# Kernel optimization log

Measured on AMD Instinct MI355X. Metric: run time of the kernel, lower is better.

The kernel has to match this reference:

```python
import jax, jax.numpy as jnp
import numpy as np

HIDDEN = 32
N_BLOCKS = 2


def setup_inputs() -> dict:
    key = jax.random.key(0)
    ks = jax.random.split(key, 8)
    B, S, F = 256, 4096, 8
    H = HIDDEN
    inp = {
        "x": jax.random.normal(ks[0], (B, S, F), dtype=jnp.float32),
        # embed
        "W_embed": jax.random.normal(ks[1], (F, H), dtype=jnp.float32) * (F ** -0.5),
        "b_embed": jnp.zeros((H,), jnp.float32),
        # per-block selective-SSM params (stacked over blocks)
        "W_delta": jax.random.normal(ks[2], (N_BLOCKS, H, H), dtype=jnp.float32) * (H ** -0.5),
        "b_delta": jnp.zeros((N_BLOCKS, H), jnp.float32),
        "A_log": jnp.log(jnp.broadcast_to(jnp.arange(1, H + 1, dtype=jnp.float32), (N_BLOCKS, H))),
        "W_gate": jax.random.normal(ks[3], (N_BLOCKS, H, H), dtype=jnp.float32) * (H ** -0.5),
        "b_gate": jnp.zeros((N_BLOCKS, H), jnp.float32),
        # head: LayerNorm + MLP
        "ln_gamma": jnp.ones((H,), jnp.float32),
        "ln_beta": jnp.zeros((H,), jnp.float32),
        "W1": jax.random.normal(ks[4], (H, H), dtype=jnp.float32) * (H ** -0.5),
        "b1": jnp.zeros((H,), jnp.float32),
        "W2": jax.random.normal(ks[5], (H, 1), dtype=jnp.float32) * (H ** -0.5),
        "b2": jnp.zeros((1,), jnp.float32),
    }
    return inp


def _ssm_block(h, Wd, bd, A_log, Wg, bg):
    """Diagonal selective SSM: input-dependent decay, gated output, residual."""
    # h: [B, S, H]
    delta = jax.nn.softplus(jnp.einsum('bsh,hk->bsk', h, Wd) + bd)  # [B,S,H]
    abar = jnp.exp(delta * (-jnp.exp(A_log)))                       # [B,S,H] in (0,1)
    xin = delta * h                                                 # [B,S,H]

    def step(s, ab_xi):
        ab, xi = ab_xi
        s = ab * s + xi
        return s, s

    B, S, H = h.shape
    s0 = jnp.zeros((B, H), h.dtype)
    # scan over time (axis S), vectorized over batch & channels
    _, states = jax.lax.scan(step, s0, (abar.transpose(1, 0, 2), xin.transpose(1, 0, 2)))
    states = states.transpose(1, 0, 2)  # [B,S,H]
    gate = jax.nn.sigmoid(jnp.einsum('bsh,hk->bsk', h, Wg) + bg)
    return h + states * gate


def reference(x, W_embed, b_embed, W_delta, b_delta, A_log, W_gate, b_gate,
              ln_gamma, ln_beta, W1, b1, W2, b2):
    h = jnp.einsum('bsf,fh->bsh', x, W_embed) + b_embed  # [B,S,H]
    for i in range(N_BLOCKS):
        h = _ssm_block(h, W_delta[i], b_delta[i], A_log[i], W_gate[i], b_gate[i])
    hl = h[:, -1, :]  # [B,H] last timestep
    mu = jnp.mean(hl, axis=-1, keepdims=True)
    var = jnp.mean((hl - mu) ** 2, axis=-1, keepdims=True)
    hn = (hl - mu) / jnp.sqrt(var + 1e-5) * ln_gamma + ln_beta
    z = jax.nn.gelu(hn @ W1 + b1)
    return (z @ W2 + b2).squeeze(-1)  # [B]
```

## Files before the change

kernel.cpp:

```cpp
#include <hip/hip_runtime.h>
#include <math.h>

#define BB 256
#define SS 4096
#define FF 8
#define HH 32
#define TT 256
#define NT (SS/TT)
#define NTHREADS 1024
#define NG 16
#define CL 16
#define SUB 8

#define L2E  1.4426950408889634f
#define LN2f 0.6931471805599453f

typedef _Float16 half2v __attribute__((ext_vector_type(2)));
typedef __fp16   pk16   __attribute__((ext_vector_type(2)));

__device__ __forceinline__ float fexp2(float x){
#if __has_builtin(__builtin_amdgcn_exp2f)
    return __builtin_amdgcn_exp2f(x);
#else
    return exp2f(x);
#endif
}
__device__ __forceinline__ float flog2(float x){
#if __has_builtin(__builtin_amdgcn_logf)
    return __builtin_amdgcn_logf(x);
#else
    return log2f(x);
#endif
}
__device__ __forceinline__ float frcp(float x){
#if __has_builtin(__builtin_amdgcn_rcpf)
    return __builtin_amdgcn_rcpf(x);
#else
    return 1.0f/x;
#endif
}
__device__ __forceinline__ float fdot2(half2v a, half2v b, float c){
#if __has_builtin(__builtin_amdgcn_fdot2)
    return __builtin_amdgcn_fdot2(a, b, c, false);
#else
    return c + (float)a.x*(float)b.x + (float)a.y*(float)b.y;
#endif
}
__device__ __forceinline__ half2v bch2(unsigned int u){
    return __builtin_bit_cast(half2v, u);
}

__device__ __forceinline__ float softplus_n(float z){
    const float t = fexp2(-fabsf(z) * L2E);
    return fmaxf(z, 0.f) + LN2f * flog2(1.f + t);
}
__device__ __forceinline__ float sigmoid_n(float z){
    return frcp(1.f + fexp2(-z * L2E));
}

__global__ __launch_bounds__(NTHREADS, 4)
void forecast_fused(const float* __restrict__ x,
                    const float* __restrict__ Wemb, const float* __restrict__ bemb,
                    const float* __restrict__ Wd,   const float* __restrict__ bd,
                    const float* __restrict__ Alog,
                    const float* __restrict__ Wg,   const float* __restrict__ bg,
                    const float* __restrict__ gmma, const float* __restrict__ beta,
                    const float* __restrict__ W1,   const float* __restrict__ b1,
                    const float* __restrict__ W2,   const float* __restrict__ b2,
                    float* __restrict__ out)
{
    __shared__ __align__(16) unsigned int xs16[2][TT][4];
    __shared__ __align__(16) unsigned int h1h[TT][16];
    __shared__ float wdpS[FF][HH];
    __shared__ float wgpS[FF][HH];
    __shared__ float bdpS[HH], bgpS[HH];
    __shared__ float2 cfS[2][NG][HH];
    __shared__ float s1s[2][HH];
    __shared__ float hlast[HH];

    const int tid = threadIdx.x;
    const int c   = tid & (HH - 1);
    const int s   = (tid >> 5) & 1;
    const int g   = tid >> 6;
    const int b   = blockIdx.x;
    const int tsb = g * CL + s * SUB;
    const int xrow = tid >> 2, xdc = tid & 3;

    if (tid < FF * HH) {
        const int f = tid >> 5, cc = tid & 31;
        float accd = 0.f, accg = 0.f;
#pragma unroll
        for (int k = 0; k < HH; ++k) {
            const float w = Wemb[f * HH + k];
            accd += w * Wd[k * HH + cc];
            accg += w * Wg[k * HH + cc];
        }
        wdpS[f][cc] = accd;
        wgpS[f][cc] = accg;
    }
    if (tid < HH) {
        float ad = bd[tid], ag = bg[tid];
#pragma unroll
        for (int k = 0; k < HH; ++k) {
            ad += bemb[k] * Wd[k * HH + tid];
            ag += bemb[k] * Wg[k * HH + tid];
        }
        bdpS[tid] = ad; bgpS[tid] = ag;
        s1s[0][tid] = 0.f;
    }
    __syncthreads();

    half2v weh[FF/2], wdh[FF/2], wgh[FF/2], wh[HH/2];
#pragma unroll
    for (int j = 0; j < FF/2; ++j) {
        half2v a;
        a.x = (_Float16)Wemb[(2*j) * HH + c];   a.y = (_Float16)Wemb[(2*j+1) * HH + c];
        weh[j] = a;
        a.x = (_Float16)wdpS[2*j][c];           a.y = (_Float16)wdpS[2*j+1][c];
        wdh[j] = a;
        a.x = (_Float16)wgpS[2*j][c];           a.y = (_Float16)wgpS[2*j+1][c];
        wgh[j] = a;
    }
#pragma unroll
    for (int j = 0; j < HH/2; ++j) {
        half2v a;
        a.x = (_Float16)Wd[HH * HH + (2*j)   * HH + c];
        a.y = (_Float16)Wd[HH * HH + (2*j+1) * HH + c];
        wh[j] = a;
    }
    const float bec  = bemb[c];
    const float bd1p = bdpS[c], bg1p = bgpS[c], bd2 = bd[HH + c];
    const float nA1 = -expf(Alog[c]) * L2E;
    const float nA2 = -expf(Alog[HH + c]) * L2E;

    float s2v = 0.f;

    {
        const float2 xv = *reinterpret_cast<const float2*>(
            x + ((size_t)b * SS + xrow) * FF + xdc * 2);
        const pk16 pk = __builtin_amdgcn_cvt_pkrtz(xv.x, xv.y);
        xs16[0][xrow][xdc] = __builtin_bit_cast(unsigned int, pk);
    }
    __syncthreads();

    for (int it = 0; it < NT; ++it) {
        const int p = it & 1;

        float2 xnext;
        if (it + 1 < NT)
            xnext = *reinterpret_cast<const float2*>(
                x + ((size_t)b * SS + (it + 1) * TT + xrow) * FF + xdc * 2);

        float prefA[SUB], loc[SUB], gtv[SUB], h0r[SUB], h1r[SUB];
        float sp = 1.f, sl = 0.f;
#pragma unroll
        for (int r = 0; r < SUB; ++r) {
            const int ts = tsb + r;
            const uint4 xq = *reinterpret_cast<const uint4*>(&xs16[p][ts][0]);
            float h0 = bec, zd = bd1p, zg = bg1p;
            h0 = fdot2(bch2(xq.x), weh[0], h0);
            h0 = fdot2(bch2(xq.y), weh[1], h0);
            h0 = fdot2(bch2(xq.z), weh[2], h0);
            h0 = fdot2(bch2(xq.w), weh[3], h0);
            zd = fdot2(bch2(xq.x), wdh[0], zd);
            zd = fdot2(bch2(xq.y), wdh[1], zd);
            zd = fdot2(bch2(xq.z), wdh[2], zd);
            zd = fdot2(bch2(xq.w), wdh[3], zd);
            zg = fdot2(bch2(xq.x), wgh[0], zg);
            zg = fdot2(bch2(xq.y), wgh[1], zg);
            zg = fdot2(bch2(xq.z), wgh[2], zg);
            zg = fdot2(bch2(xq.w), wgh[3], zg);
            const float delta = softplus_n(zd);
            const float ab    = fexp2(delta * nA1);
            sl = ab * sl + delta * h0;
            sp *= ab;
            prefA[r] = sp;
            loc[r]   = sl;
            gtv[r]   = sigmoid_n(zg);
            h0r[r]   = h0;
        }
        const float spO = __shfl_xor(sp, 32);
        const float slO = __shfl_xor(sl, 32);
        if (s) cfS[p][g][c] = make_float2(spO * sp, sp * slO + sl);
        __syncthreads();

        float cy = s1s[p][c];
#pragma unroll
        for (int ch = 0; ch < NG; ++ch) {
            const float2 ax = cfS[p][ch][c];
            const float t = ax.x * cy + ax.y;
            cy = (ch < g) ? t : cy;
        }
        const float ci = s ? (slO + spO * cy) : cy;
        if (g == NG - 1 && s) s1s[p ^ 1][c] = sl + sp * ci;

#pragma unroll
        for (int r = 0; r < SUB; ++r) {
            const float st = loc[r] + prefA[r] * ci;
            const float h1 = h0r[r] + st * gtv[r];
            h1r[r] = h1;
            const float pn = __shfl_xor(h1, 1);
            if (!(c & 1)) {
                const pk16 pk = __builtin_amdgcn_cvt_pkrtz(h1, pn);
                h1h[tsb + r][c >> 1] = __builtin_bit_cast(unsigned int, pk);
            }
        }
        if (it == NT - 1 && g == NG - 1 && s) hlast[c] = h1r[SUB - 1];
        __syncthreads();

        float sp2 = 1.f, sl2 = 0.f;
#pragma unroll
        for (int r = 0; r < SUB; ++r) {
            const uint4* rp = reinterpret_cast<const uint4*>(&h1h[tsb + r][0]);
            const uint4 q0 = rp[0], q1 = rp[1], q2 = rp[2], q3 = rp[3];
            float za = bd2, zb = 0.f;
            za = fdot2(bch2(q0.x), wh[0],  za);
            zb = fdot2(bch2(q0.y), wh[1],  zb);
            za = fdot2(bch2(q0.z), wh[2],  za);
            zb = fdot2(bch2(q0.w), wh[3],  zb);
            za = fdot2(bch2(q1.x), wh[4],  za);
            zb = fdot2(bch2(q1.y), wh[5],  zb);
            za = fdot2(bch2(q1.z), wh[6],  za);
            zb = fdot2(bch2(q1.w), wh[7],  zb);
            za = fdot2(bch2(q2.x), wh[8],  za);
            zb = fdot2(bch2(q2.y), wh[9],  zb);
            za = fdot2(bch2(q2.z), wh[10], za);
            zb = fdot2(bch2(q2.w), wh[11], zb);
            za = fdot2(bch2(q3.x), wh[12], za);
            zb = fdot2(bch2(q3.y), wh[13], zb);
            za = fdot2(bch2(q3.z), wh[14], za);
            zb = fdot2(bch2(q3.w), wh[15], zb);
            const float zd    = za + zb;
            const float delta = softplus_n(zd);
            const float ab    = fexp2(delta * nA2);
            sl2 = ab * sl2 + delta * h1r[r];
            sp2 *= ab;
        }
        const float spO2 = __shfl_xor(sp2, 32);
        const float slO2 = __shfl_xor(sl2, 32);
        if (s) cfS[p][g][c] = make_float2(spO2 * sp2, sp2 * slO2 + sl2);
        if (it + 1 < NT) {
            const pk16 pk = __builtin_amdgcn_cvt_pkrtz(xnext.x, xnext.y);
            xs16[p ^ 1][xrow][xdc] = __builtin_bit_cast(unsigned int, pk);
        }
        __syncthreads();

        if (tid < HH) {
            float cy2 = s2v;
#pragma unroll
            for (int ch = 0; ch < NG; ++ch) {
                const float2 ax = cfS[p][ch][tid];
                cy2 = ax.x * cy2 + ax.y;
            }
            s2v = cy2;
        }
    }
    __syncthreads();

    if (tid < HH) {
        float zg = bg[HH + tid];
#pragma unroll
        for (int k = 0; k < HH; ++k) zg += hlast[k] * Wg[HH * HH + k * HH + tid];
        const float gt2 = sigmoid_n(zg);
        const float h2  = hlast[tid] + s2v * gt2;

        float sum = h2;
#pragma unroll
        for (int m = 1; m < HH; m <<= 1) sum += __shfl_xor(sum, m);
        const float mu = sum * (1.0f / HH);
        const float d  = h2 - mu;
        float vs = d * d;
#pragma unroll
        for (int m = 1; m < HH; m <<= 1) vs += __shfl_xor(vs, m);
        const float rstd = rsqrtf(vs * (1.0f / HH) + 1e-5f);
        const float hn   = d * rstd * gmma[tid] + beta[tid];

        float z = b1[tid];
#pragma unroll
        for (int k = 0; k < HH; ++k) z += __shfl(hn, k) * W1[k * HH + tid];
        const float u  = 2.0f * L2E * 0.7978845608028654f * (z + 0.044715f * z * z * z);
        const float e  = fexp2(u);
        const float th = 1.f - 2.f * frcp(1.f + e);
        const float ge = 0.5f * z * (1.0f + th);
        float v = ge * W2[tid];
#pragma unroll
        for (int m = 1; m < HH; m <<= 1) v += __shfl_xor(v, m);
        if (tid == 0) out[b] = v + b2[0];
    }
}

extern "C" void kernel_launch(void* const* d_in, const int* in_sizes, int n_in,
                              void* d_out, int out_size, void* d_ws, size_t ws_size,
                              hipStream_t stream) {
    const float* x    = (const float*)d_in[0];
    const float* Wemb = (const float*)d_in[1];
    const float* bemb = (const float*)d_in[2];
    const float* Wd   = (const float*)d_in[3];
    const float* bd   = (const float*)d_in[4];
    const float* Alog = (const float*)d_in[5];
    const float* Wg   = (const float*)d_in[6];
    const float* bg   = (const float*)d_in[7];
    const float* gmma = (const float*)d_in[8];
    const float* beta = (const float*)d_in[9];
    const float* W1   = (const float*)d_in[10];
    const float* b1   = (const float*)d_in[11];
    const float* W2   = (const float*)d_in[12];
    const float* b2   = (const float*)d_in[13];
    float* out = (float*)d_out;

    forecast_fused<<<dim3(BB), dim3(NTHREADS), 0, stream>>>(
        x, Wemb, bemb, Wd, bd, Alog, Wg, bg, gmma, beta, W1, b1, W2, b2, out);
}
```

Measured before the change: 181.8 us.

## Use MFMA 16x16x32 for projections and remap wave lanes to channel-time tiles

Replaces the per-thread fdot2 projections (embed, delta, gate, and block-2 delta) with MFMA 16x16x32 f16 instructions, so each wave now handles 16 timesteps for all 32 channels. Each lane holds 4 consecutive timesteps per channel half, and the intra-wave scan combines across lane groups with shuffles. A separate cf2S buffer is added, which removes one barrier per tile because block-2 carries no longer overwrite block-1 carries. The cost is more shuffle traffic and zero-padded MFMA operands, since K is only 8 for the first projections.

```diff
diff --git a/kernel.cpp b/kernel.cpp
--- a/kernel.cpp
+++ b/kernel.cpp
@@ -9,14 +9,14 @@
 #define NT (SS/TT)
 #define NTHREADS 1024
 #define NG 16
-#define CL 16
-#define SUB 8
+#define CLR 16
 
 #define L2E  1.4426950408889634f
 #define LN2f 0.6931471805599453f
 
-typedef _Float16 half2v __attribute__((ext_vector_type(2)));
-typedef __fp16   pk16   __attribute__((ext_vector_type(2)));
+typedef _Float16 f16x8 __attribute__((ext_vector_type(8)));
+typedef float    f32x4 __attribute__((ext_vector_type(4)));
+typedef __fp16   pk16  __attribute__((ext_vector_type(2)));
 
 __device__ __forceinline__ float fexp2(float x){
 #if __has_builtin(__builtin_amdgcn_exp2f)
@@ -38,16 +38,6 @@
 #else
     return 1.0f/x;
 #endif
-}
-__device__ __forceinline__ float fdot2(half2v a, half2v b, float c){
-#if __has_builtin(__builtin_amdgcn_fdot2)
-    return __builtin_amdgcn_fdot2(a, b, c, false);
-#else
-    return c + (float)a.x*(float)b.x + (float)a.y*(float)b.y;
-#endif
-}
-__device__ __forceinline__ half2v bch2(unsigned int u){
-    return __builtin_bit_cast(half2v, u);
 }
 
 __device__ __forceinline__ float softplus_n(float z){
@@ -75,16 +65,20 @@
     __shared__ float wgpS[FF][HH];
     __shared__ float bdpS[HH], bgpS[HH];
     __shared__ float2 cfS[2][NG][HH];
+    __shared__ float2 cf2S[2][NG][HH];
     __shared__ float s1s[2][HH];
     __shared__ float hlast[HH];
 
-    const int tid = threadIdx.x;
-    const int c   = tid & (HH - 1);
-    const int s   = (tid >> 5) & 1;
-    const int g   = tid >> 6;
-    const int b   = blockIdx.x;
-    const int tsb = g * CL + s * SUB;
+    const int tid  = threadIdx.x;
+    const int lane = tid & 63;
+    const int g    = tid >> 6;
+    const int c0   = lane & 15;
+    const int grp  = lane >> 4;
+    const int r0   = grp * 4;
+    const int cb   = g * CLR;
+    const int b    = blockIdx.x;
     const int xrow = tid >> 2, xdc = tid & 3;
+    const int lm16 = (lane - 16) & 63, lm32 = (lane - 32) & 63;
 
     if (tid < FF * HH) {
         const int f = tid >> 5, cc = tid & 31;
@@ -110,28 +104,24 @@
     }
     __syncthreads();
 
-    half2v weh[FF/2], wdh[FF/2], wgh[FF/2], wh[HH/2];
-#pragma unroll
-    for (int j = 0; j < FF/2; ++j) {
-        half2v a;
-        a.x = (_Float16)Wemb[(2*j) * HH + c];   a.y = (_Float16)Wemb[(2*j+1) * HH + c];
-        weh[j] = a;
-        a.x = (_Float16)wdpS[2*j][c];           a.y = (_Float16)wdpS[2*j+1][c];
-        wdh[j] = a;
-        a.x = (_Float16)wgpS[2*j][c];           a.y = (_Float16)wgpS[2*j+1][c];
-        wgh[j] = a;
-    }
-#pragma unroll
-    for (int j = 0; j < HH/2; ++j) {
-        half2v a;
-        a.x = (_Float16)Wd[HH * HH + (2*j)   * HH + c];
-        a.y = (_Float16)Wd[HH * HH + (2*j+1) * HH + c];
-        wh[j] = a;
-    }
-    const float bec  = bemb[c];
-    const float bd1p = bdpS[c], bg1p = bgpS[c], bd2 = bd[HH + c];
-    const float nA1 = -expf(Alog[c]) * L2E;
-    const float nA2 = -expf(Alog[HH + c]) * L2E;
+    f16x8 bh0[2], bzd[2], bzg[2], bwd2[2];
+    float bec[2], bd1p[2], bg1p[2], bd2c[2], nA1[2], nA2[2];
+#pragma unroll
+    for (int q = 0; q < 2; ++q) {
+        const int cq = c0 + 16 * q;
+#pragma unroll
+        for (int j = 0; j < 8; ++j) {
+            bh0[q][j] = (lane < 16) ? (_Float16)Wemb[j * HH + cq] : (_Float16)0.f;
+            bzd[q][j] = (lane < 16) ? (_Float16)wdpS[j][cq]       : (_Float16)0.f;
+            bzg[q][j] = (lane < 16) ? (_Float16)wgpS[j][cq]       : (_Float16)0.f;
+            bwd2[q][j] = (_Float16)Wd[HH * HH + (grp * 8 + j) * HH + cq];
+        }
+        bec[q]  = bemb[cq];
+        bd1p[q] = bdpS[cq]; bg1p[q] = bgpS[cq];
+        bd2c[q] = bd[HH + cq];
+        nA1[q] = -expf(Alog[cq]) * L2E;
+        nA2[q] = -expf(Alog[HH + cq]) * L2E;
+    }
 
     float s2v = 0.f;
 
@@ -146,110 +136,144 @@
     for (int it = 0; it < NT; ++it) {
         const int p = it & 1;
 
-        float2 xnext;
+        float2 xnext = make_float2(0.f, 0.f);
         if (it + 1 < NT)
             xnext = *reinterpret_cast<const float2*>(
                 x + ((size_t)b * SS + (it + 1) * TT + xrow) * FF + xdc * 2);
 
-        float prefA[SUB], loc[SUB], gtv[SUB], h0r[SUB], h1r[SUB];
-        float sp = 1.f, sl = 0.f;
-#pragma unroll
-        for (int r = 0; r < SUB; ++r) {
-            const int ts = tsb + r;
-            const uint4 xq = *reinterpret_cast<const uint4*>(&xs16[p][ts][0]);
-            float h0 = bec, zd = bd1p, zg = bg1p;
-            h0 = fdot2(bch2(xq.x), weh[0], h0);
-            h0 = fdot2(bch2(xq.y), weh[1], h0);
-            h0 = fdot2(bch2(xq.z), weh[2], h0);
-            h0 = fdot2(bch2(xq.w), weh[3], h0);
-            zd = fdot2(bch2(xq.x), wdh[0], zd);
-            zd = fdot2(bch2(xq.y), wdh[1], zd);
-            zd = fdot2(bch2(xq.z), wdh[2], zd);
-            zd = fdot2(bch2(xq.w), wdh[3], zd);
-            zg = fdot2(bch2(xq.x), wgh[0], zg);
-            zg = fdot2(bch2(xq.y), wgh[1], zg);
-            zg = fdot2(bch2(xq.z), wgh[2], zg);
-            zg = fdot2(bch2(xq.w), wgh[3], zg);
-            const float delta = softplus_n(zd);
-            const float ab    = fexp2(delta * nA1);
-            sl = ab * sl + delta * h0;
-            sp *= ab;
-            prefA[r] = sp;
-            loc[r]   = sl;
-            gtv[r]   = sigmoid_n(zg);
-            h0r[r]   = h0;
-        }
-        const float spO = __shfl_xor(sp, 32);
-        const float slO = __shfl_xor(sl, 32);
-        if (s) cfS[p][g][c] = make_float2(spO * sp, sp * slO + sl);
+        uint4 aw = make_uint4(0u, 0u, 0u, 0u);
+        if (lane < 16) aw = *reinterpret_cast<const uint4*>(&xs16[p][cb + c0][0]);
+        const f16x8 a1 = __builtin_bit_cast(f16x8, aw);
+        f32x4 vh0[2], vzd[2], vzg[2];
+#pragma unroll
+        for (int q = 0; q < 2; ++q) {
+            f32x4 cin;
+            cin[0] = cin[1] = cin[2] = cin[3] = bec[q];
+            vh0[q] = __builtin_amdgcn_mfma_f32_16x16x32_f16(a1, bh0[q], cin, 0, 0, 0);
+            cin[0] = cin[1] = cin[2] = cin[3] = bd1p[q];
+            vzd[q] = __builtin_amdgcn_mfma_f32_16x16x32_f16(a1, bzd[q], cin, 0, 0, 0);
+            cin[0] = cin[1] = cin[2] = cin[3] = bg1p[q];
+            vzg[q] = __builtin_amdgcn_mfma_f32_16x16x32_f16(a1, bzg[q], cin, 0, 0, 0);
+        }
+
+        float pA[2][4], pl[2][4], gt[2][4], h1v[2][4];
+#pragma unroll
+        for (int q = 0; q < 2; ++q) {
+            float sp = 1.f, sl = 0.f;
+#pragma unroll
+            for (int j = 0; j < 4; ++j) {
+                const float delta = softplus_n(vzd[q][j]);
+                const float ab    = fexp2(delta * nA1[q]);
+                sl = ab * sl + delta * vh0[q][j];
+                sp *= ab;
+                pA[q][j] = sp; pl[q][j] = sl;
+                gt[q][j] = sigmoid_n(vzg[q][j]);
+            }
+        }
+        float P[2], S[2];
+        P[0] = pA[0][3]; S[0] = pl[0][3];
+        P[1] = pA[1][3]; S[1] = pl[1][3];
+#pragma unroll
+        for (int q = 0; q < 2; ++q) {
+            float Pm = __shfl(P[q], lm16), Sm = __shfl(S[q], lm16);
+            if (grp >= 1) { S[q] = P[q] * Sm + S[q]; P[q] = P[q] * Pm; }
+            float Pm2 = __shfl(P[q], lm32), Sm2 = __shfl(S[q], lm32);
+            if (grp >= 2) { S[q] = P[q] * Sm2 + S[q]; P[q] = P[q] * Pm2; }
+        }
+        if (grp == 3) {
+            cfS[p][g][c0]      = make_float2(P[0], S[0]);
+            cfS[p][g][c0 + 16] = make_float2(P[1], S[1]);
+        }
         __syncthreads();
 
-        float cy = s1s[p][c];
+        const int chc = lane & 31;
+        float cy = s1s[p][chc];
 #pragma unroll
         for (int ch = 0; ch < NG; ++ch) {
-            const float2 ax = cfS[p][ch][c];
+            const float2 ax = cfS[p][ch][chc];
             const float t = ax.x * cy + ax.y;
             cy = (ch < g) ? t : cy;
         }
-        const float ci = s ? (slO + spO * cy) : cy;
-        if (g == NG - 1 && s) s1s[p ^ 1][c] = sl + sp * ci;
-
-#pragma unroll
-        for (int r = 0; r < SUB; ++r) {
-            const float st = loc[r] + prefA[r] * ci;
-            const float h1 = h0r[r] + st * gtv[r];
-            h1r[r] = h1;
-            const float pn = __shfl_xor(h1, 1);
-            if (!(c & 1)) {
-                const pk16 pk = __builtin_amdgcn_cvt_pkrtz(h1, pn);
-                h1h[tsb + r][c >> 1] = __builtin_bit_cast(unsigned int, pk);
-            }
-        }
-        if (it == NT - 1 && g == NG - 1 && s) hlast[c] = h1r[SUB - 1];
-        __syncthreads();
-
-        float sp2 = 1.f, sl2 = 0.f;
-#pragma unroll
-        for (int r = 0; r < SUB; ++r) {
-            const uint4* rp = reinterpret_cast<const uint4*>(&h1h[tsb + r][0]);
-            const uint4 q0 = rp[0], q1 = rp[1], q2 = rp[2], q3 = rp[3];
-            float za = bd2, zb = 0.f;
-            za = fdot2(bch2(q0.x), wh[0],  za);
-            zb = fdot2(bch2(q0.y), wh[1],  zb);
-            za = fdot2(bch2(q0.z), wh[2],  za);
-            zb = fdot2(bch2(q0.w), wh[3],  zb);
-            za = fdot2(bch2(q1.x), wh[4],  za);
-            zb = fdot2(bch2(q1.y), wh[5],  zb);
-            za = fdot2(bch2(q1.z), wh[6],  za);
-            zb = fdot2(bch2(q1.w), wh[7],  zb);
-            za = fdot2(bch2(q2.x), wh[8],  za);
-            zb = fdot2(bch2(q2.y), wh[9],  zb);
-            za = fdot2(bch2(q2.z), wh[10], za);
-            zb = fdot2(bch2(q2.w), wh[11], zb);
-            za = fdot2(bch2(q3.x), wh[12], za);
-            zb = fdot2(bch2(q3.y), wh[13], zb);
-            za = fdot2(bch2(q3.z), wh[14], za);
-            zb = fdot2(bch2(q3.w), wh[15], zb);
-            const float zd    = za + zb;
-            const float delta = softplus_n(zd);
-            const float ab    = fexp2(delta * nA2);
-            sl2 = ab * sl2 + delta * h1r[r];
-            sp2 *= ab;
-        }
-        const float spO2 = __shfl_xor(sp2, 32);
-        const float slO2 = __shfl_xor(sl2, 32);
-        if (s) cfS[p][g][c] = make_float2(spO2 * sp2, sp2 * slO2 + sl2);
+        if (g == NG - 1 && lane < 32) {
+            const float2 aL = cfS[p][NG - 1][chc];
+            s1s[p ^ 1][chc] = aL.x * cy + aL.y;
+        }
+        const float cyq0 = __shfl(cy, c0);
+        const float cyq1 = __shfl(cy, c0 + 16);
+        float gin[2];
+#pragma unroll
+        for (int q = 0; q < 2; ++q) {
+            float Pe = __shfl(P[q], lm16), Se = __shfl(S[q], lm16);
+            if (grp == 0) { Pe = 1.f; Se = 0.f; }
+            gin[q] = Se + Pe * (q ? cyq1 : cyq0);
+        }
+
+#pragma unroll
+        for (int q = 0; q < 2; ++q)
+#pragma unroll
+            for (int j = 0; j < 4; ++j) {
+                const float st = pl[q][j] + pA[q][j] * gin[q];
+                h1v[q][j] = vh0[q][j] + st * gt[q][j];
+            }
+#pragma unroll
+        for (int j = 0; j < 4; ++j) {
+            const float p0 = __shfl_xor(h1v[0][j], 1);
+            const float p1 = __shfl_xor(h1v[1][j], 1);
+            unsigned int w;
+            if (lane & 1) {
+                const pk16 pk = __builtin_amdgcn_cvt_pkrtz(p1, h1v[1][j]);
+                w = __builtin_bit_cast(unsigned int, pk);
+            } else {
+                const pk16 pk = __builtin_amdgcn_cvt_pkrtz(h1v[0][j], p0);
+                w = __builtin_bit_cast(unsigned int, pk);
+            }
+            h1h[cb + r0 + j][(c0 >> 1) + ((lane & 1) ? 8 : 0)] = w;
+        }
+        if (it == NT - 1 && g == NG - 1 && grp == 3) {
+            hlast[c0]      = h1v[0][3];
+            hlast[c0 + 16] = h1v[1][3];
+        }
+
+        const uint4 aw2 = *reinterpret_cast<const uint4*>(&h1h[cb + c0][grp * 4]);
+        const f16x8 a2 = __builtin_bit_cast(f16x8, aw2);
+        float P2[2], S2[2];
+#pragma unroll
+        for (int q = 0; q < 2; ++q) {
+            f32x4 cin;
+            cin[0] = cin[1] = cin[2] = cin[3] = bd2c[q];
+            const f32x4 vd2 = __builtin_amdgcn_mfma_f32_16x16x32_f16(a2, bwd2[q], cin, 0, 0, 0);
+            float sp = 1.f, sl = 0.f;
+#pragma unroll
+            for (int j = 0; j < 4; ++j) {
+                const float delta = softplus_n(vd2[j]);
+                const float ab    = fexp2(delta * nA2[q]);
+                sl = ab * sl + delta * h1v[q][j];
+                sp *= ab;
+            }
+            P2[q] = sp; S2[q] = sl;
+        }
+#pragma unroll
+        for (int q = 0; q < 2; ++q) {
+            float Pm = __shfl(P2[q], lm16), Sm = __shfl(S2[q], lm16);
+            if (grp >= 1) { S2[q] = P2[q] * Sm + S2[q]; P2[q] = P2[q] * Pm; }
+            float Pm2 = __shfl(P2[q], lm32), Sm2 = __shfl(S2[q], lm32);
+            if (grp >= 2) { S2[q] = P2[q] * Sm2 + S2[q]; P2[q] = P2[q] * Pm2; }
+        }
+        if (grp == 3) {
+            cf2S[p][g][c0]      = make_float2(P2[0], S2[0]);
+            cf2S[p][g][c0 + 16] = make_float2(P2[1], S2[1]);
+        }
         if (it + 1 < NT) {
             const pk16 pk = __builtin_amdgcn_cvt_pkrtz(xnext.x, xnext.y);
             xs16[p ^ 1][xrow][xdc] = __builtin_bit_cast(unsigned int, pk);
         }
         __syncthreads();
 
-        if (tid < HH) {
+        if (tid < 32) {
             float cy2 = s2v;
 #pragma unroll
             for (int ch = 0; ch < NG; ++ch) {
-                const float2 ax = cfS[p][ch][tid];
+                const float2 ax = cf2S[p][ch][tid];
                 cy2 = ax.x * cy2 + ax.y;
             }
             s2v = cy2;
```

Result: faster. 167.0 us (-8.1%).
